# Kernel tuning notes

Measured on AMD Instinct MI355X. Metric: run time of the kernel, lower is better.

The kernel has to match this reference:

```python
import jax, jax.numpy as jnp
import numpy as np

# Straight-through sign binarization (Binarize in BNN code mutates .data, so
# autograd sees identity -> custom_vjp with identity backward).
@jax.custom_vjp
def binarize(x):
    return jnp.sign(x)

def _bin_fwd(x):
    return jnp.sign(x), None

def _bin_bwd(_, g):
    return (g,)

binarize.defvjp(_bin_fwd, _bin_bwd)

EPS = 1e-5  # torch BatchNorm1d default eps

def batchnorm(x, g, b):
    # training-mode BN: batch statistics, biased variance
    if x.ndim == 3:  # (N, C, L): stats over N and L
        m = x.mean(axis=(0, 2), keepdims=True)
        v = x.var(axis=(0, 2), keepdims=True)
        return (x - m) / jnp.sqrt(v + EPS) * g[None, :, None] + b[None, :, None]
    m = x.mean(axis=0)
    v = x.var(axis=0)
    return (x - m) / jnp.sqrt(v + EPS) * g + b

def hardtanh(x):
    return jnp.clip(x, -1.0, 1.0)

def maxpool3(x):
    # MaxPool1d(kernel=3, stride=3): trim then reshape-max
    N, C, L = x.shape
    Lp = L // 3
    return x[:, :, :Lp * 3].reshape(N, C, Lp, 3).max(axis=-1)

def bconv(x, w, b, binarize_input=True):
    # BinarizeConv1d: kernel 41, dilation 2, VALID padding; weights sign-binarized,
    # inputs binarized except when in_channels == 3 (first layer rule in BNN code).
    xb = binarize(x) if binarize_input else x
    wb = binarize(w)
    y = jax.lax.conv_general_dilated(
        xb, wb, window_strides=(1,), padding='VALID',
        rhs_dilation=(2,), dimension_numbers=('NCH', 'OIH', 'NCH'))
    return y + b[None, :, None]

def blinear(x, w, b):
    # BinarizeLinear: in_features 832/1024 != 784 -> binarize input and weight
    return binarize(x) @ binarize(w).T + b

def _forward(x, bn0_g, bn0_b, conv1_w, conv1_b, bn1_g, bn1_b,
             conv2_w, conv2_b, bn2_g, bn2_b, conv3_w, conv3_b,
             bn3_g, bn3_b, conv4_w, conv4_b, bn4_g, bn4_b,
             conv5_w, conv5_b, fc1_w, fc1_b, bn5_g, bn5_b,
             fc2_w, fc2_b, bn6_g, bn6_b):
    h = hardtanh(batchnorm(x, bn0_g, bn0_b))
    h = maxpool3(bconv(h, conv1_w, conv1_b, binarize_input=False))  # (N,64,5306)
    h = hardtanh(batchnorm(h, bn1_g, bn1_b))
    h = maxpool3(bconv(h, conv2_w, conv2_b))  # (N,64,1742)
    h = hardtanh(batchnorm(h, bn2_g, bn2_b))
    h = maxpool3(bconv(h, conv3_w, conv3_b))  # (N,64,554)
    h = hardtanh(batchnorm(h, bn3_g, bn3_b))
    h = maxpool3(bconv(h, conv4_w, conv4_b))  # (N,64,158)
    h = hardtanh(batchnorm(h, bn4_g, bn4_b))
    h = maxpool3(bconv(h, conv5_w, conv5_b))  # (N,32,26)
    h = h.reshape(-1, 16 * 52)                # (N, 832)
    h = hardtanh(batchnorm(blinear(h, fc1_w, fc1_b), bn5_g, bn5_b))
    h = batchnorm(blinear(h, fc2_w, fc2_b), bn6_g, bn6_b)
    return jax.nn.log_softmax(h, axis=1)

def setup_inputs() -> dict:
    key = jax.random.key(0)
    ks = jax.random.split(key, 32)
    def rn(k, shape, s=0.1):
        return jax.random.normal(k, shape, dtype=jnp.float32) * s
    def bn_params(kg, kb, c):
        return 1.0 + rn(kg, (c,)), rn(kb, (c,))
    N, L, K = 64, 16000, 41
    d = {"x": jax.random.normal(ks[0], (N, 3, L), dtype=jnp.float32)}
    d["bn0_g"], d["bn0_b"] = bn_params(ks[1], ks[2], 3)
    d["conv1_w"], d["conv1_b"] = rn(ks[3], (64, 3, K)), rn(ks[4], (64,), 0.01)
    d["bn1_g"], d["bn1_b"] = bn_params(ks[5], ks[6], 64)
    d["conv2_w"], d["conv2_b"] = rn(ks[7], (64, 64, K)), rn(ks[8], (64,), 0.01)
    d["bn2_g"], d["bn2_b"] = bn_params(ks[9], ks[10], 64)
    d["conv3_w"], d["conv3_b"] = rn(ks[11], (64, 64, K)), rn(ks[12], (64,), 0.01)
    d["bn3_g"], d["bn3_b"] = bn_params(ks[13], ks[14], 64)
    d["conv4_w"], d["conv4_b"] = rn(ks[15], (64, 64, K)), rn(ks[16], (64,), 0.01)
    d["bn4_g"], d["bn4_b"] = bn_params(ks[17], ks[18], 64)
    d["conv5_w"], d["conv5_b"] = rn(ks[19], (32, 64, K)), rn(ks[20], (32,), 0.01)
    d["fc1_w"], d["fc1_b"] = rn(ks[21], (1024, 832)), rn(ks[22], (1024,), 0.01)
    d["bn5_g"], d["bn5_b"] = bn_params(ks[23], ks[24], 1024)
    d["fc2_w"], d["fc2_b"] = rn(ks[25], (1000, 1024)), rn(ks[26], (1000,), 0.01)
    d["bn6_g"], d["bn6_b"] = bn_params(ks[27], ks[28], 1000)
    return d

def reference(x, bn0_g, bn0_b, conv1_w, conv1_b, bn1_g, bn1_b,
              conv2_w, conv2_b, bn2_g, bn2_b, conv3_w, conv3_b,
              bn3_g, bn3_b, conv4_w, conv4_b, bn4_g, bn4_b,
              conv5_w, conv5_b, fc1_w, fc1_b, bn5_g, bn5_b,
              fc2_w, fc2_b, bn6_g, bn6_b):
    return _forward(x, bn0_g, bn0_b, conv1_w, conv1_b, bn1_g, bn1_b,
                    conv2_w, conv2_b, bn2_g, bn2_b, conv3_w, conv3_b,
                    bn3_g, bn3_b, conv4_w, conv4_b, bn4_g, bn4_b,
                    conv5_w, conv5_b, fc1_w, fc1_b, bn5_g, bn5_b,
                    fc2_w, fc2_b, bn6_g, bn6_b)
```

## Files before the change

### kernel.cpp

```cpp
#include <hip/hip_runtime.h>
#include <hip/hip_bf16.h>
#include <stdint.h>

typedef __hip_bfloat16 bf16;
typedef unsigned long long u64;
typedef unsigned short u16;

typedef __attribute__((ext_vector_type(8))) short bf16x8;
typedef __attribute__((ext_vector_type(4))) float f32x4;
typedef __attribute__((ext_vector_type(4))) int i32x4;

#define FIXCAP (1u << 20)

static __device__ __forceinline__ float ldin(const void* p, long i, int f32) {
    return f32 ? ((const float*)p)[i] : __bfloat162float(((const bf16*)p)[i]);
}

__global__ void k_probe(const void* x, unsigned* ctl) {
    int tid = threadIdx.x;
    int good = 0;
    for (int i = tid; i < 1024; i += 256) {
        float v = __bfloat162float(((const bf16*)x)[2 * i]);
        float a = fabsf(v);
        if (v == 0.0f || (isfinite(v) && a >= 1e-4f && a <= 100.0f)) good++;
    }
    __shared__ int s[256];
    s[tid] = good; __syncthreads();
    for (int st = 128; st > 0; st >>= 1) {
        if (tid < st) s[tid] += s[tid + st];
        __syncthreads();
    }
    if (tid == 0) { ctl[0] = 0u; ctl[1] = (s[0] >= 700) ? 0u : 1u; }
}

__global__ void k_sentinel(void* outv, const unsigned* ctl, float val) {
    int i = blockIdx.x * 256 + threadIdx.x;
    if (i >= 64000) return;
    if (ctl[1]) ((float*)outv)[i] = val;
    else ((bf16*)outv)[i] = __float2bfloat16(val);
}

__device__ __forceinline__ void pack_convw_task(const void* w, uint2* wp, int Co, int f32,
                                                int bx, int tid) {
    int t = bx * 256 + tid;
    if (t >= Co * 41) return;
    int co = t / 41, k = t % 41;
    unsigned w0 = 0, w1 = 0;
    for (int c = 0; c < 32; c++)
        if (ldin(w, (co * 64 + c) * 41 + k, f32) > 0.f) w0 |= (1u << c);
    for (int c = 0; c < 32; c++)
        if (ldin(w, (co * 64 + 32 + c) * 41 + k, f32) > 0.f) w1 |= (1u << c);
    wp[t] = make_uint2(w0, w1);
}
__device__ __forceinline__ void pack_rows_task(const void* w, unsigned* wp, int rows, int F,
                                               int f32, int bx, int tid) {
    int Fw = F >> 5;
    int t = bx * 256 + tid;
    if (t >= rows * Fw) return;
    int r = t / Fw, wi = t % Fw;
    unsigned m = 0;
    for (int j = 0; j < 32; j++)
        if (ldin(w, (long)r * F + wi * 32 + j, f32) > 0.f) m |= (1u << j);
    wp[t] = m;
}

__global__ void k_prep(const void* x, const void* c1w, const void* c2w, const void* c3w,
                       const void* c4w, const void* c5w, const void* f1w, const void* f2w,
                       u16* afrag, signed char* af2, uint2* w3p, uint2* w4p, uint2* w5p,
                       unsigned* fc1wp, unsigned* fc2wp, u64* stats, double* part0,
                       const unsigned* ctl) {
    int f32 = ctl[1];
    int task = blockIdx.y, bx = blockIdx.x, tid = threadIdx.x;
    switch (task) {
        case 0: {
            int t = bx * 256 + tid;
            if (t < 2304) {
                int m = t / 576, rem = t - m * 576;
                int ks = rem / 64, lane = rem - ks * 64;
                int li = lane & 15, hq = lane >> 4;
                int row = 16 * m + li;
                int g = 4 * ks + hq;
                int c = g / 11, t0 = 4 * (g - 11 * c);
                u16* outp = afrag + (size_t)t * 8;
                for (int i2 = 0; i2 < 4; i2++) {
                    int tt = t0 + i2;
                    u16 sv = 0;
                    if (g < 33 && tt <= 40) {
                        float wv = ldin(c1w, (row * 3 + c) * 41 + tt, f32);
                        sv = (wv > 0.f) ? (u16)0x3F80 : ((wv < 0.f) ? (u16)0xBF80 : (u16)0);
                    }
                    outp[2 * i2] = sv;
                    outp[2 * i2 + 1] = sv;
                }
            }
        } break;
        case 1: {
            int t = bx * 256 + tid;
            if (t < 11264) {
                int lane = t & 63, g = t >> 6;
                int m = g & 3, tt = g >> 2;
                int li = lane & 15, hq = lane >> 4;
                int co = 16 * m + li;
                unsigned dws[4];
#pragma unroll
                for (int dw = 0; dw < 4; dw++) {
                    unsigned v = 0;
                    if (tt <= 40) {
#pragma unroll
                        for (int b = 0; b < 4; b++) {
                            int c = 16 * hq + 4 * dw + b;
                            float wv = ldin(c2w, (co * 64 + c) * 41 + tt, f32);
                            unsigned byte = (wv > 0.f) ? 0x01u : 0xFFu;
                            v |= byte << (8 * b);
                        }
                    }
                    dws[dw] = v;
                }
                ((uint4*)af2)[t] = make_uint4(dws[0], dws[1], dws[2], dws[3]);
            }
        } break;
        case 2: pack_convw_task(c3w, w3p, 64, f32, bx, tid); break;
        case 3: pack_convw_task(c4w, w4p, 64, f32, bx, tid); break;
        case 4: pack_convw_task(c5w, w5p, 32, f32, bx, tid); break;
        case 5: pack_rows_task(f1w, fc1wp, 1024, 832, f32, bx, tid); break;
        case 6: pack_rows_task(f2w, fc2wp, 1000, 1024, f32, bx, tid); break;
        case 7: {
            int i = bx * 256 + tid;
            if (i < 14400) stats[i] = 0ull;
        } break;
        case 8: {
            if (bx >= 96) return;
            int c = bx >> 5, s = bx & 31;
            double s1 = 0, s2 = 0;
            for (int n = 0; n < 64; n++) {
                long base = (long)(n * 3 + c) * 16000;
                for (int l = s * 256 + tid; l < 16000; l += 32 * 256) {
                    double v = (double)ldin(x, base + l, f32);
                    s1 += v; s2 += v * v;
                }
            }
            __shared__ double a1[256], a2[256];
            a1[tid] = s1; a2[tid] = s2;
            __syncthreads();
            for (int st = 128; st > 0; st >>= 1) {
                if (tid < st) { a1[tid] += a1[tid + st]; a2[tid] += a2[tid + st]; }
                __syncthreads();
            }
            if (tid == 0) { part0[(c * 32 + s) * 2] = a1[0]; part0[(c * 32 + s) * 2 + 1] = a2[0]; }
        } break;
    }
}

__global__ __launch_bounds__(256, 3) void k_conv1(const void* __restrict__ x,
                                                  const double* __restrict__ part0,
                                                  const void* __restrict__ g0,
                                                  const void* __restrict__ b0,
                                                  const u16* __restrict__ afrag,
                                                  double* __restrict__ yb,
                                                  const void* __restrict__ g1,
                                                  const void* __restrict__ b1,
                                                  uint2* __restrict__ x2p,
                                                  unsigned* __restrict__ fixcnt,
                                                  unsigned* __restrict__ fixlist,
                                                  const unsigned* __restrict__ ctl,
                                                  int pass) {
    __shared__ unsigned xs[8][140];
    __shared__ float pool[4][48][20];
    __shared__ double sbuf[4][64][2];
    __shared__ unsigned char sb[4][16][64];
    __shared__ double2 pqs[64];
    __shared__ float2 b0f[3];
    int f32 = ctl[1];
    int n = blockIdx.y, bx = blockIdx.x, tid = threadIdx.x;
    if (tid < 3) {
        int c = tid;
        double s1 = 0, s2 = 0;
        for (int s = 0; s < 32; s++) { s1 += part0[(c * 32 + s) * 2]; s2 += part0[(c * 32 + s) * 2 + 1]; }
        double M = 64.0 * 16000.0;
        double mu = s1 / M, var = s2 / M - mu * mu;
        double A = (double)ldin(g0, c, f32) / sqrt(var + 1e-5);
        b0f[c] = make_float2((float)A, (float)((double)ldin(b0, c, f32) - mu * A));
    }
    if (pass && tid >= 64 && tid < 128) {
        int c = tid - 64;
        double s1 = 0, s2 = 0;
        for (int s = 0; s < 16; s++) { s1 += yb[(c * 16 + s) * 2]; s2 += yb[(c * 16 + s) * 2 + 1]; }
        double M = 64.0 * 5306.0;
        double mu = s1 / M, var = s2 / M - mu * mu;
        double A = (double)ldin(g1, c, f32) / sqrt(var + 1e-5);
        pqs[c] = make_double2(A, (double)ldin(b1, c, f32) - mu * A);
    }
    __syncthreads();

    unsigned* xsf = &xs[0][0];
    for (int f = tid; f < 1120; f += 256) {
        int rc = f / 140, qi = f - rc * 140;
        int r = rc >> 2, c = rc & 3;
        unsigned dw = 0u;
        if (c < 3) {
            int xpos = 192 * bx + 2 * qi + r;
            if (xpos < 16000) {
                float2 pb = b0f[c];
                float v = fmaf(ldin(x, (long)(n * 3 + c) * 16000 + xpos, f32), pb.x, pb.y);
                v = fminf(fmaxf(v, -1.f), 1.f);
                bf16 h = __float2bfloat16(v);
                float hf = __bfloat162float(h);
                bf16 lo = __float2bfloat16(v - hf);
                dw = (unsigned)__bfloat16_as_ushort(h) | ((unsigned)__bfloat16_as_ushort(lo) << 16);
            }
        }
        xsf[f] = dw;
    }
    __syncthreads();

    int lane = tid & 63;
    int li = lane & 15, hq = lane >> 4;
    int w = __builtin_amdgcn_readfirstlane(tid >> 6);

    f32x4 zz = {0.f, 0.f, 0.f, 0.f};
    f32x4 acc[4][3];
#pragma unroll
    for (int m = 0; m < 4; m++)
#pragma unroll
        for (int nf = 0; nf < 3; nf++) acc[m][nf] = zz;

    int boff[3];
#pragma unroll
    for (int nf = 0; nf < 3; nf++) {
        int pl = 48 * w + 16 * nf + li;
        boff[nf] = (pl & 1) * 560 + (pl >> 1);
    }

    const bf16x8* ag = (const bf16x8*)afrag;
#pragma unroll 1
    for (int ks = 0; ks < 9; ks++) {
        int g = 4 * ks + hq;
        int c = g / 11;
        int kb = c * 140 + 4 * (g - 11 * c);
        bf16x8 a0 = ag[(0 * 9 + ks) * 64 + lane];
        bf16x8 a1 = ag[(1 * 9 + ks) * 64 + lane];
        bf16x8 a2 = ag[(2 * 9 + ks) * 64 + lane];
        bf16x8 a3 = ag[(3 * 9 + ks) * 64 + lane];
#pragma unroll
        for (int nf = 0; nf < 3; nf++) {
            const unsigned* bp = xsf + boff[nf] + kb;
            union { int4 i4; bf16x8 v; } u;
            u.i4 = make_int4(bp[0], bp[1], bp[2], bp[3]);
            acc[0][nf] = __builtin_amdgcn_mfma_f32_16x16x32_bf16(a0, u.v, acc[0][nf], 0, 0, 0);
            acc[1][nf] = __builtin_amdgcn_mfma_f32_16x16x32_bf16(a1, u.v, acc[1][nf], 0, 0, 0);
            acc[2][nf] = __builtin_amdgcn_mfma_f32_16x16x32_bf16(a2, u.v, acc[2][nf], 0, 0, 0);
            acc[3][nf] = __builtin_amdgcn_mfma_f32_16x16x32_bf16(a3, u.v, acc[3][nf], 0, 0, 0);
        }
    }

    int lp0 = 64 * bx + 16 * w;
    if (pass == 0) {
#pragma unroll
        for (int m = 0; m < 4; m++) {
#pragma unroll
            for (int nf = 0; nf < 3; nf++)
                *(f32x4*)&pool[w][16 * nf + li][4 * hq] = acc[m][nf];
            double s = 0.0, q = 0.0;
#pragma unroll
            for (int i = 0; i < 4; i++) {
                int pc = hq + 4 * i;
                float mq = fmaxf(fmaxf(pool[w][3 * pc][li], pool[w][3 * pc + 1][li]),
                                 pool[w][3 * pc + 2][li]);
                if (lp0 + pc < 5306) {
                    double d = (double)mq;
                    s += d; q += d * d;
                }
            }
            s += __shfl_down(s, 32, 64); s += __shfl_down(s, 16, 64);
            q += __shfl_down(q, 32, 64); q += __shfl_down(q, 16, 64);
            if (lane < 16) { sbuf[w][16 * m + lane][0] = s; sbuf[w][16 * m + lane][1] = q; }
        }
        __syncthreads();
        if (tid < 64) {
            double s = sbuf[0][tid][0] + sbuf[1][tid][0] + sbuf[2][tid][0] + sbuf[3][tid][0];
            double q = sbuf[0][tid][1] + sbuf[1][tid][1] + sbuf[2][tid][1] + sbuf[3][tid][1];
            int sbk = bx & 15;
            atomicAdd(&yb[(tid * 16 + sbk) * 2], s);
            atomicAdd(&yb[(tid * 16 + sbk) * 2 + 1], q);
        }
    } else {
#pragma unroll
        for (int m = 0; m < 4; m++) {
#pragma unroll
            for (int nf = 0; nf < 3; nf++)
                *(f32x4*)&pool[w][16 * nf + li][4 * hq] = acc[m][nf];
            int c = 16 * m + li;
            double2 P = pqs[c];
            double athr = 2e-3 * fabs(P.x);
#pragma unroll
            for (int i = 0; i < 4; i++) {
                int pc = hq + 4 * i;
                int lp = lp0 + pc;
                float mq = fmaxf(fmaxf(pool[w][3 * pc][li], pool[w][3 * pc + 1][li]),
                                 pool[w][3 * pc + 2][li]);
                if (lp < 5306) {
                    double v = (double)mq * P.x + P.y;
                    sb[w][pc][c] = (v > 0.0) ? 1 : 0;
                    if (fabs(v) < athr) {
                        unsigned idx = atomicAdd(fixcnt, 1u);
                        if (idx < FIXCAP)
                            fixlist[idx] = ((unsigned)n << 19) | ((unsigned)c << 13) | (unsigned)lp;
                    }
                }
            }
        }
        __syncthreads();
        if (tid < 64) {
            int lp = 64 * bx + tid;
            if (lp < 5306) {
                const unsigned* sp = (const unsigned*)&sb[tid >> 4][tid & 15][0];
                unsigned w0 = 0, w1 = 0;
#pragma unroll
                for (int jw = 0; jw < 8; jw++)
                    w0 |= (((sp[jw] * 0x01020408u) >> 24) & 0xFu) << (4 * jw);
#pragma unroll
                for (int jw = 8; jw < 16; jw++)
                    w1 |= (((sp[jw] * 0x01020408u) >> 24) & 0xFu) << (4 * (jw - 8));
                x2p[(size_t)n * 5306 + lp] = make_uint2(w0, w1);
            }
        }
    }
}

__global__ void k_fix(const unsigned* __restrict__ fixcnt, const unsigned* __restrict__ fixlist,
                      const double* __restrict__ yb, const void* g1, const void* b1,
                      const void* __restrict__ x, const void* __restrict__ c1w,
                      const double* __restrict__ part0, const void* g0, const void* b0,
                      unsigned* __restrict__ x2p, const unsigned* __restrict__ ctl) {
    int f32 = ctl[1];
    unsigned cnt = min(*fixcnt, FIXCAP);
    for (unsigned t = blockIdx.x * 256 + threadIdx.x; t < cnt; t += gridDim.x * 256) {
        unsigned e = fixlist[t];
        int n = e >> 19, c = (e >> 13) & 63, l = e & 8191;
        double s1 = 0, s2 = 0;
        for (int s = 0; s < 16; s++) { s1 += yb[(c * 16 + s) * 2]; s2 += yb[(c * 16 + s) * 2 + 1]; }
        double M = 64.0 * 5306.0;
        double mu = s1 / M, var = s2 / M - mu * mu;
        double A = (double)ldin(g1, c, f32) / sqrt(var + 1e-5);
        double B = (double)ldin(b1, c, f32) - mu * A;
        double best = -1e300;
        for (int r = 0; r < 3; r++) {
            int pp = 3 * l + r;
            double acc = 0.0;
            for (int cc = 0; cc < 3; cc++) {
                double p1 = 0, p2 = 0;
                for (int s = 0; s < 32; s++) { p1 += part0[(cc * 32 + s) * 2]; p2 += part0[(cc * 32 + s) * 2 + 1]; }
                double M0 = 64.0 * 16000.0;
                double mu0 = p1 / M0, var0 = p2 / M0 - mu0 * mu0;
                double A0 = (double)ldin(g0, cc, f32) / sqrt(var0 + 1e-5);
                double B0 = (double)ldin(b0, cc, f32) - mu0 * A0;
                for (int k = 0; k < 41; k++) {
                    float wf = ldin(c1w, (c * 3 + cc) * 41 + k, f32);
                    double sgn = (wf > 0.f) ? 1.0 : ((wf < 0.f) ? -1.0 : 0.0);
                    double xv = (double)ldin(x, (long)(n * 3 + cc) * 16000 + pp + 2 * k, f32);
                    xv = fmin(fmax(xv * A0 + B0, -1.0), 1.0);
                    acc = fma(sgn, xv, acc);
                }
            }
            best = fmax(best, acc);
        }
        double v = best * A + B;
        unsigned* word = &x2p[((size_t)n * 5306 + l) * 2 + (c >> 5)];
        unsigned bit = 1u << (c & 31);
        if (v > 0.0) atomicOr(word, bit);
        else atomicAnd(word, ~bit);
    }
}

__global__ __launch_bounds__(256, 3) void k_conv_i8(const uint2* __restrict__ xp,
                                                    const signed char* __restrict__ af2,
                                                    u16* __restrict__ mout,
                                                    u64* __restrict__ stat) {
    __shared__ __align__(16) char arena[24576];
    unsigned* xsd = (unsigned*)arena;
    int n = blockIdx.y, bx = blockIdx.x, tid = threadIdx.x;
    int base = 192 * bx;

    for (int e = tid; e < 272; e += 256) {
        int pos = base + e;
        int r = e & 1, qi = e >> 1;
        unsigned* dst = xsd + (r * 136 + qi) * 20;
        unsigned d[16];
        if (pos < 5306) {
            uint2 mk = xp[(size_t)n * 5306 + pos];
#pragma unroll
            for (int dw = 0; dw < 8; dw++) {
                unsigned nib = (mk.x >> (4 * dw)) & 0xFu;
                unsigned sp = (nib * 0x00204081u) & 0x01010101u;
                d[dw] = ~(sp * 0xFEu);
            }
#pragma unroll
            for (int dw = 0; dw < 8; dw++) {
                unsigned nib = (mk.y >> (4 * dw)) & 0xFu;
                unsigned sp = (nib * 0x00204081u) & 0x01010101u;
                d[8 + dw] = ~(sp * 0xFEu);
            }
        } else {
#pragma unroll
            for (int dw = 0; dw < 16; dw++) d[dw] = 0u;
        }
#pragma unroll
        for (int v4 = 0; v4 < 4; v4++)
            *(uint4*)(dst + 4 * v4) = make_uint4(d[4 * v4], d[4 * v4 + 1],
                                                 d[4 * v4 + 2], d[4 * v4 + 3]);
    }
    __syncthreads();

    int lane = tid & 63;
    int li = lane & 15, hq = lane >> 4;
    int w = __builtin_amdgcn_readfirstlane(tid >> 6);

    i32x4 zz = {0, 0, 0, 0};
    i32x4 acc[4][3];
#pragma unroll
    for (int m = 0; m < 4; m++)
#pragma unroll
        for (int nf = 0; nf < 3; nf++) acc[m][nf] = zz;

    int boff[3];
#pragma unroll
    for (int nf = 0; nf < 3; nf++) {
        int pl = 48 * w + 16 * nf + li;
        boff[nf] = ((pl & 1) * 136 + (pl >> 1)) * 80 + 16 * hq;
    }

    const i32x4* ag = (const i32x4*)af2;
    const char* xsb = (const char*)xsd;

#pragma unroll
    for (int t = 0; t < 41; t++) {
        i32x4 a0 = ag[(t * 4 + 0) * 64 + lane];
        i32x4 a1 = ag[(t * 4 + 1) * 64 + lane];
        i32x4 a2 = ag[(t * 4 + 2) * 64 + lane];
        i32x4 a3 = ag[(t * 4 + 3) * 64 + lane];
#pragma unroll
        for (int nf = 0; nf < 3; nf++) {
            i32x4 b = *(const i32x4*)(xsb + boff[nf] + t * 80);
            acc[0][nf] = __builtin_amdgcn_mfma_i32_16x16x64_i8(a0, b, acc[0][nf], 0, 0, 0);
            acc[1][nf] = __builtin_amdgcn_mfma_i32_16x16x64_i8(a1, b, acc[1][nf], 0, 0, 0);
            acc[2][nf] = __builtin_amdgcn_mfma_i32_16x16x64_i8(a2, b, acc[2][nf], 0, 0, 0);
            acc[3][nf] = __builtin_amdgcn_mfma_i32_16x16x64_i8(a3, b, acc[3][nf], 0, 0, 0);
        }
    }

    __syncthreads();
    int (*pooli)[48][20] = (int (*)[48][20])arena;
    u16 (*mt)[72] = (u16 (*)[72])(arena + 15360);
    int sbk = bx & 15;
#pragma unroll
    for (int m = 0; m < 4; m++) {
#pragma unroll
        for (int nf = 0; nf < 3; nf++)
            *(i32x4*)&pooli[w][16 * nf + li][4 * hq] = acc[m][nf];
        int c = 16 * m + li;
        unsigned s = 0, q = 0;
#pragma unroll
        for (int i = 0; i < 4; i++) {
            int pc = hq + 4 * i;
            int d = max(max(pooli[w][3 * pc][li], pooli[w][3 * pc + 1][li]),
                        pooli[w][3 * pc + 2][li]);
            int mv = (2624 - d) >> 1;
            mt[c][16 * w + pc] = (u16)mv;
            int lp = 64 * bx + 16 * w + pc;
            if (lp < 1742) {
                s += (unsigned)mv;
                q += (unsigned)(mv * mv);
            }
        }
        s += __shfl_down(s, 32, 64); s += __shfl_down(s, 16, 64);
        q += __shfl_down(q, 32, 64); q += __shfl_down(q, 16, 64);
        if (lane < 16) {
            atomicAdd(&stat[((16 * m + lane) * 16 + sbk) * 2], (u64)s);
            atomicAdd(&stat[((16 * m + lane) * 16 + sbk) * 2 + 1], (u64)q);
        }
    }
    __syncthreads();
    {
        int c = tid >> 2, seg = tid & 3;
        int lp0 = 64 * bx + seg * 16;
        size_t rowb = ((size_t)n * 64 + c) * 1742;
        const u16* mp = &mt[c][seg * 16];
        if (lp0 + 15 < 1742) {
            unsigned* op = (unsigned*)(mout + rowb + lp0);
#pragma unroll
            for (int j = 0; j < 8; j++)
                op[j] = (unsigned)mp[2 * j] | ((unsigned)mp[2 * j + 1] << 16);
        } else {
            for (int j = 0; j < 16; j++) {
                int lp = lp0 + j;
                if (lp < 1742) mout[rowb + lp] = mp[j];
            }
        }
    }
}

__global__ __launch_bounds__(256) void k_conv_binm(const u16* __restrict__ min_,
                                                   const u64* __restrict__ statIn,
                                                   const void* g, const void* b, double M,
                                                   const uint2* __restrict__ wp,
                                                   u16* __restrict__ mout,
                                                   u64* __restrict__ statOut,
                                                   int Lp, int Lin, int Co,
                                                   const unsigned* __restrict__ ctl) {
    __shared__ double2 pqs[64];
    __shared__ uint2 xt[272];
    int f32 = ctl[1];
    int n = blockIdx.y, tid = threadIdx.x;
    if (tid < 64) {
        int c = tid;
        u64 s1 = 0, s2 = 0;
        for (int s = 0; s < 16; s++) { s1 += statIn[(c * 16 + s) * 2]; s2 += statIn[(c * 16 + s) * 2 + 1]; }
        double mu = (double)s1 / M;
        double varm = (double)s2 / M - mu * mu;
        double A = (double)ldin(g, c, f32) / sqrt(4.0 * varm + 1e-5);
        pqs[c] = make_double2(-2.0 * A, 2.0 * A * mu + (double)ldin(b, c, f32));
    }
    __syncthreads();
    int base = blockIdx.x * 192;
    for (int i = tid; i < 272; i += 256) {
        int pos = base + i;
        unsigned w0 = 0, w1 = 0;
        if (pos < Lin) {
            const u16* mp = min_ + (size_t)n * 64 * Lin + pos;
#pragma unroll 4
            for (int c = 0; c < 32; c++) {
                double2 p = pqs[c];
                if ((double)mp[(size_t)c * Lin] * p.x + p.y > 0.0) w0 |= 1u << c;
            }
#pragma unroll 4
            for (int c = 0; c < 32; c++) {
                double2 p = pqs[c + 32];
                if ((double)mp[(size_t)(c + 32) * Lin] * p.x + p.y > 0.0) w1 |= 1u << c;
            }
        }
        xt[i] = make_uint2(w0, w1);
    }
    __syncthreads();

    int lane = tid & 63;
    int wave = __builtin_amdgcn_readfirstlane(tid >> 6);
    int co0 = blockIdx.z * 32 + wave * 8;
    int lp = blockIdx.x * 64 + lane;

    int acc[8][3] = {};
    uint2 xa = xt[3 * lane];
    for (int k = 0; k < 41; k++) {
        uint2 xb = xt[3 * lane + 2 * k + 1];
        uint2 xc = xt[3 * lane + 2 * k + 2];
#pragma unroll
        for (int j = 0; j < 8; j++) {
            uint2 w = wp[(co0 + j) * 41 + k];
            acc[j][0] += __popc(w.x ^ xa.x) + __popc(w.y ^ xa.y);
            acc[j][1] += __popc(w.x ^ xb.x) + __popc(w.y ^ xb.y);
            acc[j][2] += __popc(w.x ^ xc.x) + __popc(w.y ^ xc.y);
        }
        xa = xc;
    }
    bool ok = lp < Lp;
    int sb = blockIdx.x & 15;
#pragma unroll
    for (int j = 0; j < 8; j++) {
        int m = min(min(acc[j][0], acc[j][1]), acc[j][2]);
        if (ok) mout[((size_t)n * 64 + co0 + j) * Lp + lp] = (u16)m;
        if (statOut) {
            unsigned s = ok ? (unsigned)m : 0u;
            unsigned q = ok ? (unsigned)(m * m) : 0u;
            for (int off = 32; off > 0; off >>= 1) {
                s += __shfl_down(s, off, 64);
                q += __shfl_down(q, off, 64);
            }
            if (lane == 0) {
                atomicAdd(&statOut[((co0 + j) * 16 + sb) * 2], (u64)s);
                atomicAdd(&statOut[((co0 + j) * 16 + sb) * 2 + 1], (u64)q);
            }
        }
    }
}

__global__ void k_c5fc1(const u16* __restrict__ m4, const u64* __restrict__ s4,
                        const void* g4, const void* b4,
                        const uint2* __restrict__ w5p, const void* __restrict__ b5,
                        const unsigned* __restrict__ fc1wp, u16* __restrict__ acc1,
                        u64* __restrict__ s5, const unsigned* __restrict__ ctl) {
    __shared__ double2 pqs[64];
    __shared__ uint2 xt[280];
    __shared__ int m5s[32][26];
    __shared__ unsigned xw[26];
    int f32 = ctl[1];
    int n = blockIdx.x, tid = threadIdx.x;
    const int Lin = 158;
    if (tid < 64) {
        int c = tid;
        u64 s1 = 0, s2 = 0;
        for (int s = 0; s < 16; s++) { s1 += s4[(c * 16 + s) * 2]; s2 += s4[(c * 16 + s) * 2 + 1]; }
        double M = 64.0 * 158.0;
        double mu = (double)s1 / M;
        double varm = (double)s2 / M - mu * mu;
        double A = (double)ldin(g4, c, f32) / sqrt(4.0 * varm + 1e-5);
        pqs[c] = make_double2(-2.0 * A, 2.0 * A * mu + (double)ldin(b4, c, f32));
    }
    __syncthreads();
    for (int i = tid; i < 280; i += 256) {
        unsigned w0 = 0, w1 = 0;
        if (i < Lin) {
            const u16* mp = m4 + (size_t)n * 64 * Lin + i;
#pragma unroll 4
            for (int c = 0; c < 32; c++) {
                double2 p = pqs[c];
                if ((double)mp[(size_t)c * Lin] * p.x + p.y > 0.0) w0 |= 1u << c;
            }
#pragma unroll 4
            for (int c = 0; c < 32; c++) {
                double2 p = pqs[c + 32];
                if ((double)mp[(size_t)(c + 32) * Lin] * p.x + p.y > 0.0) w1 |= 1u << c;
            }
        }
        xt[i] = make_uint2(w0, w1);
    }
    __syncthreads();

    int lane = tid & 63;
    int wave = __builtin_amdgcn_readfirstlane(tid >> 6);
    int co0 = wave * 8;
    int acc[8][3] = {};
    uint2 xa = xt[3 * lane];
    for (int k = 0; k < 41; k++) {
        uint2 xb = xt[3 * lane + 2 * k + 1];
        uint2 xc = xt[3 * lane + 2 * k + 2];
#pragma unroll
        for (int j = 0; j < 8; j++) {
            uint2 w = w5p[(co0 + j) * 41 + k];
            acc[j][0] += __popc(w.x ^ xa.x) + __popc(w.y ^ xa.y);
            acc[j][1] += __popc(w.x ^ xb.x) + __popc(w.y ^ xb.y);
            acc[j][2] += __popc(w.x ^ xc.x) + __popc(w.y ^ xc.y);
        }
        xa = xc;
    }
    if (lane < 26) {
#pragma unroll
        for (int j = 0; j < 8; j++)
            m5s[co0 + j][lane] = min(min(acc[j][0], acc[j][1]), acc[j][2]);
    }
    __syncthreads();
    if (tid < 26) {
        unsigned mask = 0;
        for (int j = 0; j < 32; j++) {
            int f = tid * 32 + j, c = f / 26, l = f % 26;
            double yv = 2624.0 - 2.0 * (double)m5s[c][l] + (double)ldin(b5, c, f32);
            if (yv > 0.0) mask |= 1u << j;
        }
        xw[tid] = mask;
    }
    __syncthreads();
#pragma unroll
    for (int i = 0; i < 4; i++) {
        int j = tid + i * 256;
        unsigned a = 0;
        for (int w = 0; w < 26; w++) a += __popc(xw[w] ^ fc1wp[j * 26 + w]);
        acc1[n * 1024 + j] = (u16)a;
        atomicAdd(&s5[j * 2], (u64)a);
        atomicAdd(&s5[j * 2 + 1], (u64)(a * a));
    }
}

__global__ void k_fc2(const u16* __restrict__ acc1, const u64* __restrict__ s5,
                      const void* g5, const void* b5, const unsigned* __restrict__ fc2wp,
                      u16* __restrict__ acc2, u64* __restrict__ s6, const unsigned* ctl) {
    __shared__ double2 pq5s[1024];
    __shared__ unsigned xw[32];
    int f32 = ctl[1];
    int n = blockIdx.y, tid = threadIdx.x;
    for (int f = tid; f < 1024; f += 256) {
        u64 a1 = s5[f * 2], a2 = s5[f * 2 + 1];
        double mu = (double)a1 / 64.0;
        double varm = (double)a2 / 64.0 - mu * mu;
        double A = (double)ldin(g5, f, f32) / sqrt(4.0 * varm + 1e-5);
        pq5s[f] = make_double2(-2.0 * A, 2.0 * A * mu + (double)ldin(b5, f, f32));
    }
    __syncthreads();
    if (tid < 32) {
        unsigned mask = 0;
        for (int j = 0; j < 32; j++) {
            int f = tid * 32 + j;
            double2 p = pq5s[f];
            if ((double)acc1[n * 1024 + f] * p.x + p.y > 0.0) mask |= 1u << j;
        }
        xw[tid] = mask;
    }
    __syncthreads();
    int j = blockIdx.x * 256 + tid;
    if (j >= 1000) return;
    unsigned a = 0;
    for (int w = 0; w < 32; w++) a += __popc(xw[w] ^ fc2wp[j * 32 + w]);
    acc2[n * 1000 + j] = (u16)a;
    atomicAdd(&s6[j * 2], (u64)a);
    atomicAdd(&s6[j * 2 + 1], (u64)(a * a));
}

__global__ void k_lsm(const u16* __restrict__ acc2, const u64* __restrict__ s6,
                      const void* g6, const void* b6, const unsigned* ctl, void* outv) {
    int n = blockIdx.x, tid = threadIdx.x;
    int f32 = ctl[1];
    __shared__ double red[256];
    double v[4];
    double mx = -1e300;
#pragma unroll
    for (int i = 0; i < 4; i++) {
        int j = tid + i * 256;
        if (j < 1000) {
            u64 a1 = s6[j * 2], a2 = s6[j * 2 + 1];
            double mu = (double)a1 / 64.0;
            double varm = (double)a2 / 64.0 - mu * mu;
            double A = (double)ldin(g6, j, f32) / sqrt(4.0 * varm + 1e-5);
            v[i] = (double)acc2[n * 1000 + j] * (-2.0 * A) + (2.0 * A * mu + (double)ldin(b6, j, f32));
            mx = fmax(mx, v[i]);
        } else v[i] = -1e300;
    }
    red[tid] = mx; __syncthreads();
    for (int s = 128; s > 0; s >>= 1) {
        if (tid < s) red[tid] = fmax(red[tid], red[tid + s]);
        __syncthreads();
    }
    mx = red[0]; __syncthreads();
    double sum = 0.0;
#pragma unroll
    for (int i = 0; i < 4; i++) {
        int j = tid + i * 256;
        if (j < 1000) sum += exp(v[i] - mx);
    }
    red[tid] = sum; __syncthreads();
    for (int s = 128; s > 0; s >>= 1) {
        if (tid < s) red[tid] += red[tid + s];
        __syncthreads();
    }
    double ls = log(red[0]);
#pragma unroll
    for (int i = 0; i < 4; i++) {
        int j = tid + i * 256;
        if (j < 1000) {
            float r = (float)(v[i] - mx - ls);
            if (!isfinite(r)) r = -700.0f;
            if (f32) ((float*)outv)[n * 1000 + j] = r;
            else ((bf16*)outv)[n * 1000 + j] = __float2bfloat16(r);
        }
    }
}

extern "C" void kernel_launch(void* const* d_in, const int* in_sizes, int n_in,
                              void* d_out, int out_size, void* d_ws, size_t ws_size,
                              hipStream_t stream) {
    const void* x       = d_in[0];
    const void* bn0_g   = d_in[1];
    const void* bn0_b   = d_in[2];
    const void* conv1_w = d_in[3];
    const void* bn1_g   = d_in[5];
    const void* bn1_b   = d_in[6];
    const void* conv2_w = d_in[7];
    const void* bn2_g   = d_in[9];
    const void* bn2_b   = d_in[10];
    const void* conv3_w = d_in[11];
    const void* bn3_g   = d_in[13];
    const void* bn3_b   = d_in[14];
    const void* conv4_w = d_in[15];
    const void* bn4_g   = d_in[17];
    const void* bn4_b   = d_in[18];
    const void* conv5_w = d_in[19];
    const void* conv5_b = d_in[20];
    const void* fc1_w   = d_in[21];
    const void* bn5_g   = d_in[23];
    const void* bn5_b   = d_in[24];
    const void* fc2_w   = d_in[25];
    const void* bn6_g   = d_in[27];
    const void* bn6_b   = d_in[28];

    char* wsb = (char*)d_ws;
    size_t off = 0;
    auto alloc = [&](size_t bytes) -> void* {
        off = (off + 255) & ~(size_t)255;
        void* p = wsb + off;
        off += bytes;
        return p;
    };

    unsigned* ctl   = (unsigned*)alloc(256);
    unsigned* x2p   = (unsigned*)alloc(2716672);
    u16*      m2    = (u16*)alloc(14270464);
    u16*      m3    = (u16*)alloc(4538368);
    u16*      m4    = (u16*)alloc(1294336);
    u16*      acc1  = (u16*)alloc(131072);
    u16*      acc2  = (u16*)alloc(128000);
    u16*      afrag = (u16*)alloc(36864);
    signed char* af2 = (signed char*)alloc(180224);
    uint2*    w3p   = (uint2*)alloc(20992);
    uint2*    w4p   = (uint2*)alloc(20992);
    uint2*    w5p   = (uint2*)alloc(10496);
    unsigned* fc1wp = (unsigned*)alloc(106496);
    unsigned* fc2wp = (unsigned*)alloc(128000);
    u64*      stats = (u64*)alloc(14400 * 8);
    double*   part0 = (double*)alloc(2048);
    unsigned* fixlist = (unsigned*)alloc(FIXCAP * 4);
    size_t need = (off + 255) & ~(size_t)255;

    u64* s2 = stats;
    u64* s3 = stats + 2048;
    u64* s4 = stats + 4096;
    u64* s5 = stats + 6144;
    u64* s6 = stats + 8192;
    double* yb = (double*)(stats + 12288);
    unsigned* fixcnt = (unsigned*)(stats + 14340);

    k_probe<<<1, 256, 0, stream>>>(x, ctl);

    if (n_in != 29) {
        k_sentinel<<<250, 256, 0, stream>>>(d_out, ctl, -(3000.0f + (float)n_in));
        return;
    }
    if (ws_size < need) {
        k_sentinel<<<250, 256, 0, stream>>>(d_out, ctl, -1500.0f);
        return;
    }

    k_prep<<<dim3(125, 9), 256, 0, stream>>>(x, conv1_w, conv2_w, conv3_w, conv4_w, conv5_w,
                                             fc1_w, fc2_w, afrag, af2, w3p, w4p, w5p,
                                             fc1wp, fc2wp, stats, part0, ctl);

    k_conv1<<<dim3(83, 64), 256, 0, stream>>>(x, part0, bn0_g, bn0_b, afrag, yb,
                                              bn1_g, bn1_b, (uint2*)x2p,
                                              fixcnt, fixlist, ctl, 0);
    k_conv1<<<dim3(83, 64), 256, 0, stream>>>(x, part0, bn0_g, bn0_b, afrag, yb,
                                              bn1_g, bn1_b, (uint2*)x2p,
                                              fixcnt, fixlist, ctl, 1);
    k_fix<<<64, 256, 0, stream>>>(fixcnt, fixlist, yb, bn1_g, bn1_b, x, conv1_w,
                                  part0, bn0_g, bn0_b, x2p, ctl);

    k_conv_i8<<<dim3(28, 64), 256, 0, stream>>>((const uint2*)x2p, af2, m2, s2);
    k_conv_binm<<<dim3(9, 64, 2), 256, 0, stream>>>(m2, s2, bn2_g, bn2_b, 64.0 * 1742.0,
                                                    w3p, m3, s3, 554, 1742, 64, ctl);
    k_conv_binm<<<dim3(3, 64, 2), 256, 0, stream>>>(m3, s3, bn3_g, bn3_b, 64.0 * 554.0,
                                                    w4p, m4, s4, 158, 554, 64, ctl);

    k_c5fc1<<<64, 256, 0, stream>>>(m4, s4, bn4_g, bn4_b, w5p, conv5_b, fc1wp, acc1, s5, ctl);
    k_fc2<<<dim3(4, 64), 256, 0, stream>>>(acc1, s5, bn5_g, bn5_b, fc2wp, acc2, s6, ctl);
    k_lsm<<<64, 256, 0, stream>>>(acc2, s6, bn6_g, bn6_b, ctl, d_out);
}
```

Before: 776.9 us.

## Store pooled conv1 outputs once instead of recomputing conv1 in two passes

Conv1 was previously run twice, once to gather BN statistics and once to binarize and pack. Now a single conv1 pass writes the pooled float outputs to a workspace buffer alongside the statistics, and a new pack kernel applies BN1, collects near-threshold fix entries, and packs the sign bits. This removes a full recomputation of the MFMA convolution at the cost of writing and reading roughly 87 MB of float intermediates. The int8 conv2 inner loop is also software-pipelined with rotating A-fragment register buffers so loads are issued ahead of the MFMAs.

```diff
diff --git a/kernel.cpp b/kernel.cpp
--- a/kernel.cpp
+++ b/kernel.cpp
@@ -11,6 +11,7 @@
 typedef __attribute__((ext_vector_type(4))) int i32x4;
 
 #define FIXCAP (1u << 20)
+#define YQS 5312
 
 static __device__ __forceinline__ float ldin(const void* p, long i, int f32) {
     return f32 ? ((const float*)p)[i] : __bfloat162float(((const bf16*)p)[i]);
@@ -156,19 +157,13 @@
                                                   const void* __restrict__ g0,
                                                   const void* __restrict__ b0,
                                                   const u16* __restrict__ afrag,
+                                                  float* __restrict__ yq,
                                                   double* __restrict__ yb,
-                                                  const void* __restrict__ g1,
-                                                  const void* __restrict__ b1,
-                                                  uint2* __restrict__ x2p,
-                                                  unsigned* __restrict__ fixcnt,
-                                                  unsigned* __restrict__ fixlist,
-                                                  const unsigned* __restrict__ ctl,
-                                                  int pass) {
+                                                  const unsigned* __restrict__ ctl) {
     __shared__ unsigned xs[8][140];
     __shared__ float pool[4][48][20];
     __shared__ double sbuf[4][64][2];
-    __shared__ unsigned char sb[4][16][64];
-    __shared__ double2 pqs[64];
+    __shared__ float yst[16][68];
     __shared__ float2 b0f[3];
     int f32 = ctl[1];
     int n = blockIdx.y, bx = blockIdx.x, tid = threadIdx.x;
@@ -180,15 +175,6 @@
         double mu = s1 / M, var = s2 / M - mu * mu;
         double A = (double)ldin(g0, c, f32) / sqrt(var + 1e-5);
         b0f[c] = make_float2((float)A, (float)((double)ldin(b0, c, f32) - mu * A));
-    }
-    if (pass && tid >= 64 && tid < 128) {
-        int c = tid - 64;
-        double s1 = 0, s2 = 0;
-        for (int s = 0; s < 16; s++) { s1 += yb[(c * 16 + s) * 2]; s2 += yb[(c * 16 + s) * 2 + 1]; }
-        double M = 64.0 * 5306.0;
-        double mu = s1 / M, var = s2 / M - mu * mu;
-        double A = (double)ldin(g1, c, f32) / sqrt(var + 1e-5);
-        pqs[c] = make_double2(A, (double)ldin(b1, c, f32) - mu * A);
     }
     __syncthreads();
 
@@ -254,77 +240,80 @@
     }
 
     int lp0 = 64 * bx + 16 * w;
-    if (pass == 0) {
-#pragma unroll
-        for (int m = 0; m < 4; m++) {
-#pragma unroll
-            for (int nf = 0; nf < 3; nf++)
-                *(f32x4*)&pool[w][16 * nf + li][4 * hq] = acc[m][nf];
-            double s = 0.0, q = 0.0;
-#pragma unroll
-            for (int i = 0; i < 4; i++) {
-                int pc = hq + 4 * i;
-                float mq = fmaxf(fmaxf(pool[w][3 * pc][li], pool[w][3 * pc + 1][li]),
-                                 pool[w][3 * pc + 2][li]);
-                if (lp0 + pc < 5306) {
-                    double d = (double)mq;
-                    s += d; q += d * d;
-                }
-            }
-            s += __shfl_down(s, 32, 64); s += __shfl_down(s, 16, 64);
-            q += __shfl_down(q, 32, 64); q += __shfl_down(q, 16, 64);
-            if (lane < 16) { sbuf[w][16 * m + lane][0] = s; sbuf[w][16 * m + lane][1] = q; }
-        }
+#pragma unroll
+    for (int m = 0; m < 4; m++) {
+#pragma unroll
+        for (int nf = 0; nf < 3; nf++)
+            *(f32x4*)&pool[w][16 * nf + li][4 * hq] = acc[m][nf];
+        double s = 0.0, q = 0.0;
+        float mqv[4];
+#pragma unroll
+        for (int i = 0; i < 4; i++) {
+            int pc = hq + 4 * i;
+            float mq = fmaxf(fmaxf(pool[w][3 * pc][li], pool[w][3 * pc + 1][li]),
+                             pool[w][3 * pc + 2][li]);
+            mqv[i] = mq;
+            if (lp0 + pc < 5306) {
+                double d = (double)mq;
+                s += d; q += d * d;
+            }
+        }
+        s += __shfl_down(s, 32, 64); s += __shfl_down(s, 16, 64);
+        q += __shfl_down(q, 32, 64); q += __shfl_down(q, 16, 64);
+        if (lane < 16) { sbuf[w][16 * m + lane][0] = s; sbuf[w][16 * m + lane][1] = q; }
+#pragma unroll
+        for (int i = 0; i < 4; i++)
+            yst[li][16 * w + hq + 4 * i] = mqv[i];
         __syncthreads();
-        if (tid < 64) {
-            double s = sbuf[0][tid][0] + sbuf[1][tid][0] + sbuf[2][tid][0] + sbuf[3][tid][0];
-            double q = sbuf[0][tid][1] + sbuf[1][tid][1] + sbuf[2][tid][1] + sbuf[3][tid][1];
-            int sbk = bx & 15;
-            atomicAdd(&yb[(tid * 16 + sbk) * 2], s);
-            atomicAdd(&yb[(tid * 16 + sbk) * 2 + 1], q);
-        }
-    } else {
-#pragma unroll
-        for (int m = 0; m < 4; m++) {
-#pragma unroll
-            for (int nf = 0; nf < 3; nf++)
-                *(f32x4*)&pool[w][16 * nf + li][4 * hq] = acc[m][nf];
-            int c = 16 * m + li;
-            double2 P = pqs[c];
-            double athr = 2e-3 * fabs(P.x);
-#pragma unroll
-            for (int i = 0; i < 4; i++) {
-                int pc = hq + 4 * i;
-                int lp = lp0 + pc;
-                float mq = fmaxf(fmaxf(pool[w][3 * pc][li], pool[w][3 * pc + 1][li]),
-                                 pool[w][3 * pc + 2][li]);
-                if (lp < 5306) {
-                    double v = (double)mq * P.x + P.y;
-                    sb[w][pc][c] = (v > 0.0) ? 1 : 0;
-                    if (fabs(v) < athr) {
-                        unsigned idx = atomicAdd(fixcnt, 1u);
-                        if (idx < FIXCAP)
-                            fixlist[idx] = ((unsigned)n << 19) | ((unsigned)c << 13) | (unsigned)lp;
-                    }
-                }
-            }
+        {
+            int r = tid >> 4, c4 = (tid & 15) * 4;
+            float4 v = *(const float4*)&yst[r][c4];
+            *(float4*)&yq[((size_t)n * 64 + 16 * m + r) * YQS + 64 * bx + c4] = v;
         }
         __syncthreads();
-        if (tid < 64) {
-            int lp = 64 * bx + tid;
-            if (lp < 5306) {
-                const unsigned* sp = (const unsigned*)&sb[tid >> 4][tid & 15][0];
-                unsigned w0 = 0, w1 = 0;
-#pragma unroll
-                for (int jw = 0; jw < 8; jw++)
-                    w0 |= (((sp[jw] * 0x01020408u) >> 24) & 0xFu) << (4 * jw);
-#pragma unroll
-                for (int jw = 8; jw < 16; jw++)
-                    w1 |= (((sp[jw] * 0x01020408u) >> 24) & 0xFu) << (4 * (jw - 8));
-                x2p[(size_t)n * 5306 + lp] = make_uint2(w0, w1);
-            }
-        }
-    }
+    }
+    if (tid < 64) {
+        double s = sbuf[0][tid][0] + sbuf[1][tid][0] + sbuf[2][tid][0] + sbuf[3][tid][0];
+        double q = sbuf[0][tid][1] + sbuf[1][tid][1] + sbuf[2][tid][1] + sbuf[3][tid][1];
+        int sbk = bx & 15;
+        atomicAdd(&yb[(tid * 16 + sbk) * 2], s);
+        atomicAdd(&yb[(tid * 16 + sbk) * 2 + 1], q);
+    }
+}
+
+__global__ void k_pack_y(const float* __restrict__ yq, const double* __restrict__ yb,
+                         const void* g1, const void* b1,
+                         uint2* __restrict__ xp,
+                         unsigned* __restrict__ fixcnt, unsigned* __restrict__ fixlist,
+                         const unsigned* __restrict__ ctl) {
+    __shared__ double2 pqs[64];
+    int f32 = ctl[1];
+    int tid = threadIdx.x;
+    if (tid < 64) {
+        int c = tid;
+        double s1 = 0, s2 = 0;
+        for (int s = 0; s < 16; s++) { s1 += yb[(c * 16 + s) * 2]; s2 += yb[(c * 16 + s) * 2 + 1]; }
+        double M = 64.0 * 5306.0;
+        double mu = s1 / M;
+        double var = s2 / M - mu * mu;
+        double A = (double)ldin(g1, c, f32) / sqrt(var + 1e-5);
+        pqs[c] = make_double2(A, (double)ldin(b1, c, f32) - mu * A);
+    }
+    __syncthreads();
+    int n = blockIdx.y;
+    int l = blockIdx.x * 256 + tid;
+    if (l >= 5306) return;
+    unsigned w0 = 0, w1 = 0;
+    for (int c = 0; c < 64; c++) {
+        double2 p = pqs[c];
+        double v = (double)yq[((size_t)n * 64 + c) * YQS + l] * p.x + p.y;
+        if (fabs(v) < 2e-3 * fabs(p.x)) {
+            unsigned idx = atomicAdd(fixcnt, 1u);
+            if (idx < FIXCAP) fixlist[idx] = ((unsigned)n << 19) | ((unsigned)c << 13) | (unsigned)l;
+        }
+        if (v > 0.0) { if (c < 32) w0 |= 1u << c; else w1 |= 1u << (c - 32); }
+    }
+    xp[(size_t)n * 5306 + l] = make_uint2(w0, w1);
 }
 
 __global__ void k_fix(const unsigned* __restrict__ fixcnt, const unsigned* __restrict__ fixlist,
@@ -432,21 +421,31 @@
     const i32x4* ag = (const i32x4*)af2;
     const char* xsb = (const char*)xsd;
 
-#pragma unroll
-    for (int t = 0; t < 41; t++) {
-        i32x4 a0 = ag[(t * 4 + 0) * 64 + lane];
-        i32x4 a1 = ag[(t * 4 + 1) * 64 + lane];
-        i32x4 a2 = ag[(t * 4 + 2) * 64 + lane];
-        i32x4 a3 = ag[(t * 4 + 3) * 64 + lane];
-#pragma unroll
-        for (int nf = 0; nf < 3; nf++) {
-            i32x4 b = *(const i32x4*)(xsb + boff[nf] + t * 80);
-            acc[0][nf] = __builtin_amdgcn_mfma_i32_16x16x64_i8(a0, b, acc[0][nf], 0, 0, 0);
-            acc[1][nf] = __builtin_amdgcn_mfma_i32_16x16x64_i8(a1, b, acc[1][nf], 0, 0, 0);
-            acc[2][nf] = __builtin_amdgcn_mfma_i32_16x16x64_i8(a2, b, acc[2][nf], 0, 0, 0);
-            acc[3][nf] = __builtin_amdgcn_mfma_i32_16x16x64_i8(a3, b, acc[3][nf], 0, 0, 0);
-        }
-    }
+#define LOADA(B, t) { B[0] = ag[((t) * 4 + 0) * 64 + lane]; \
+                      B[1] = ag[((t) * 4 + 1) * 64 + lane]; \
+                      B[2] = ag[((t) * 4 + 2) * 64 + lane]; \
+                      B[3] = ag[((t) * 4 + 3) * 64 + lane]; }
+#define CMPT(B, t) { \
+    _Pragma("unroll") \
+    for (int nf = 0; nf < 3; nf++) { \
+        i32x4 b = *(const i32x4*)(xsb + boff[nf] + (t) * 80); \
+        acc[0][nf] = __builtin_amdgcn_mfma_i32_16x16x64_i8(B[0], b, acc[0][nf], 0, 0, 0); \
+        acc[1][nf] = __builtin_amdgcn_mfma_i32_16x16x64_i8(B[1], b, acc[1][nf], 0, 0, 0); \
+        acc[2][nf] = __builtin_amdgcn_mfma_i32_16x16x64_i8(B[2], b, acc[2][nf], 0, 0, 0); \
+        acc[3][nf] = __builtin_amdgcn_mfma_i32_16x16x64_i8(B[3], b, acc[3][nf], 0, 0, 0); \
+    } }
+
+    i32x4 A0[4], A1[4], A2[4];
+    LOADA(A0, 0); LOADA(A1, 1);
+#pragma unroll
+    for (int t3 = 0; t3 < 39; t3 += 3) {
+        LOADA(A2, t3 + 2); CMPT(A0, t3);
+        LOADA(A0, t3 + 3); CMPT(A1, t3 + 1);
+        LOADA(A1, t3 + 4); CMPT(A2, t3 + 2);
+    }
+    CMPT(A0, 39); CMPT(A1, 40);
+#undef LOADA
+#undef CMPT
 
     __syncthreads();
     int (*pooli)[48][20] = (int (*)[48][20])arena;
@@ -789,6 +788,7 @@
 
     unsigned* ctl   = (unsigned*)alloc(256);
     unsigned* x2p   = (unsigned*)alloc(2716672);
+    float*    yq    = (float*)alloc((size_t)64 * 64 * YQS * 4);
     u16*      m2    = (u16*)alloc(14270464);
     u16*      m3    = (u16*)alloc(4538368);
     u16*      m4    = (u16*)alloc(1294336);
@@ -829,12 +829,9 @@
                                              fc1_w, fc2_w, afrag, af2, w3p, w4p, w5p,
                                              fc1wp, fc2wp, stats, part0, ctl);
 
-    k_conv1<<<dim3(83, 64), 256, 0, stream>>>(x, part0, bn0_g, bn0_b, afrag, yb,
-                                              bn1_g, bn1_b, (uint2*)x2p,
-                                              fixcnt, fixlist, ctl, 0);
-    k_conv1<<<dim3(83, 64), 256, 0, stream>>>(x, part0, bn0_g, bn0_b, afrag, yb,
-                                              bn1_g, bn1_b, (uint2*)x2p,
-                                              fixcnt, fixlist, ctl, 1);
+    k_conv1<<<dim3(83, 64), 256, 0, stream>>>(x, part0, bn0_g, bn0_b, afrag, yq, yb, ctl);
+    k_pack_y<<<dim3(21, 64), 256, 0, stream>>>(yq, yb, bn1_g, bn1_b, (uint2*)x2p,
+                                               fixcnt, fixlist, ctl);
     k_fix<<<64, 256, 0, stream>>>(fixcnt, fixlist, yb, bn1_g, bn1_b, x, conv1_w,
                                   part0, bn0_g, bn0_b, x2p, ctl);
 
```

New measurement: 771.6 us. About the same (-0.7%).
